# Performance work log

Measured on AMD Instinct MI355X. Metric: run time of the kernel, lower is better.

The kernel has to match this reference:

```python
import jax, jax.numpy as jnp
import numpy as np

STRIDE = 1
PADDING = 1


def sign_ste(w):
    # forward: 2*(w>0)-1 ; backward: identity (straight-through estimator)
    s = 2.0 * (w > 0.0).astype(w.dtype) - 1.0
    return w + jax.lax.stop_gradient(s - w)


def setup_inputs() -> dict:
    key = jax.random.key(0)
    kx, kw = jax.random.split(key)
    x = jax.random.normal(kx, (32, 256, 56, 56), dtype=jnp.float32)
    # mirror torch.rand(shape) * 0.001
    weight = jax.random.uniform(kw, (256, 256, 3, 3), dtype=jnp.float32) * 0.001
    return {"x": x, "weight": weight}


def reference(x, weight):
    # per-output-channel scaling factor: mean |w| over (in, kh, kw), detached
    scaling = jnp.mean(jnp.abs(weight), axis=(1, 2, 3), keepdims=True)  # [O,1,1,1]
    scaling = jax.lax.stop_gradient(scaling)
    binary_weights = scaling * sign_ste(weight)
    y = jax.lax.conv_general_dilated(
        x, binary_weights,
        window_strides=(STRIDE, STRIDE),
        padding=[(PADDING, PADDING), (PADDING, PADDING)],
        dimension_numbers=("NCHW", "OIHW", "NCHW"),
    )
    return y
```

## Files before the change

kernel.cpp:

```cpp
#include <hip/hip_runtime.h>
#include <stdint.h>


typedef float f32x4 __attribute__((ext_vector_type(4)));

__global__ __launch_bounds__(256) void stage1U(const float* __restrict__ x,
                                               float* __restrict__ U,
                                               const float* __restrict__ w,
                                               float* __restrict__ scale,
                                               int* __restrict__ nneg,
                                               int* __restrict__ negidx) {
    __shared__ float Ls[16][64];
    __shared__ float red[4];
    __shared__ int cnt;
    const int t = threadIdx.x;
    if (blockIdx.x < 1568) {
        const int b    = blockIdx.x;
        const int n    = b / 49;
        const int tile = b - n * 49;
        const int g    = t >> 4;
        const int sl   = t & 15;
        const int hw4  = tile * 16 + sl;
        const f32x4* xp =
            (const f32x4*)(x + (size_t)(n * 256 + g * 16) * 3136) + hw4;
        f32x4 s = {0.f, 0.f, 0.f, 0.f};
#pragma unroll
        for (int c = 0; c < 16; ++c)
            s += __builtin_nontemporal_load(xp + c * 784);
        *(f32x4*)&Ls[g][sl * 4] = s;
        __syncthreads();
        if (t < 64) {
            float us = 0.f;
#pragma unroll
            for (int g2 = 0; g2 < 16; ++g2) us += Ls[g2][t];
            U[(size_t)n * 3136 + tile * 64 + t] = us;
        }
    } else {
        const int o = blockIdx.x - 1568;
        if (t == 0) cnt = 0;
        __syncthreads();
        const float* wp = w + ((size_t)o * 256 + t) * 9;
        float s = 0.f;
#pragma unroll
        for (int k = 0; k < 9; ++k) {
            const float v = wp[k];
            s += fabsf(v);
            if (v <= 0.f) {
                const int slot = atomicAdd(&cnt, 1);
                negidx[o * 2304 + slot] = t * 9 + k;
            }
        }
#pragma unroll
        for (int off = 32; off > 0; off >>= 1) s += __shfl_down(s, off);
        if ((t & 63) == 0) red[t >> 6] = s;
        __syncthreads();
        if (t == 0) {
            scale[o] = (red[0] + red[1] + red[2] + red[3]) * (1.f / 2304.f);
            nneg[o]  = cnt;
        }
    }
}

__global__ __launch_bounds__(256) void youtbox(const float* __restrict__ U,
                                               const float* __restrict__ scale,
                                               const int* __restrict__ nneg,
                                               const int* __restrict__ negidx,
                                               const float* __restrict__ x,
                                               float* __restrict__ out) {
    __shared__ float Us[3136];
    __shared__ float Tls[3136];
    __shared__ float ssc[4];
    __shared__ int   snn[4];
    const int b  = blockIdx.x;
    const int og = b & 63;
    const int n  = b >> 6;
    const int t  = threadIdx.x;

    if (t < 4) {
        ssc[t] = scale[og * 4 + t];
        snn[t] = nneg[og * 4 + t];
    }
    const f32x4* Un4 = (const f32x4*)(U + (size_t)n * 3136);
    f32x4* Us4 = (f32x4*)Us;
#pragma unroll
    for (int j = 0; j < 4; ++j) {
        const int i = t + j * 256;
        if (i < 784) Us4[i] = Un4[i];
    }
    __syncthreads();
    for (int p = t; p < 3136; p += 256) {
        const int h = p / 56, w = p - h * 56;
        float acc = 0.f;
#pragma unroll
        for (int r = -1; r <= 1; ++r) {
            const int hh = h + r;
            if (hh < 0 || hh > 55) continue;
            const float* row = Us + hh * 56;
            if (w > 0)  acc += row[w - 1];
            acc += row[w];
            if (w < 55) acc += row[w + 1];
        }
        Tls[p] = acc;
    }
    __syncthreads();

    const f32x4* T4 = (const f32x4*)Tls;
#pragma unroll
    for (int ol = 0; ol < 4; ++ol) {
        const int o = og * 4 + ol;
        const float sc = ssc[ol];
        const int nn = snn[ol];
        f32x4* op = (f32x4*)(out + ((size_t)n * 256 + o) * 3136);
        if (nn == 0) {
#pragma unroll
            for (int j = 0; j < 4; ++j) {
                const int hw4 = t + j * 256;
                if (hw4 >= 784) break;
                f32x4 v = T4[hw4] * sc;
                __builtin_nontemporal_store(v, op + hw4);
            }
        } else {
            const float c2 = 2.f * sc;
#pragma unroll
            for (int j = 0; j < 4; ++j) {
                const int hw4 = t + j * 256;
                if (hw4 >= 784) break;
                f32x4 v = T4[hw4] * sc;
                for (int q = 0; q < nn; ++q) {
                    const int iof = negidx[o * 2304 + q];
                    const int ic = iof / 9, rs = iof - ic * 9;
                    const int r = rs / 3 - 1, s2 = rs - (rs / 3) * 3 - 1;
                    const float* xpl = x + ((size_t)n * 256 + ic) * 3136;
#pragma unroll
                    for (int e = 0; e < 4; ++e) {
                        const int p = hw4 * 4 + e;
                        const int h = p / 56 + r, ww = p - (p / 56) * 56 + s2;
                        const float xv = (h >= 0 && h < 56 && ww >= 0 && ww < 56)
                                             ? xpl[h * 56 + ww] : 0.f;
                        v[e] -= c2 * xv;
                    }
                }
                __builtin_nontemporal_store(v, op + hw4);
            }
        }
    }
}

extern "C" void kernel_launch(void* const* d_in, const int* in_sizes, int n_in,
                              void* d_out, int out_size, void* d_ws, size_t ws_size,
                              hipStream_t stream) {
    const float* x = (const float*)d_in[0];
    const float* w = (const float*)d_in[1];
    float* out = (float*)d_out;

    char* ws = (char*)d_ws;
    size_t off = 0;
    float* U = (float*)(ws + off);
    off += (size_t)32 * 3136 * 4;
    float* scale = (float*)(ws + off);
    off += 256 * 4;
    int* nneg = (int*)(ws + off);
    off += 256 * 4;
    int* negidx = (int*)(ws + off);

    stage1U<<<dim3(1824), 256, 0, stream>>>(x, U, w, scale, nneg, negidx);
    youtbox<<<dim3(2048), 256, 0, stream>>>(U, scale, nneg, negidx, x, out);
}
```

Baseline: 184.8 us.

## Fuse both stages into one persistent kernel with atomic-flag dataflow sync

Merges the channel-sum/weight-stats kernel and the output kernel into a single persistent kernel of 1024 blocks. The last block finishing a batch's channel sum computes the 3x3 box-summed map T once per batch and publishes it via a release flag. Output blocks spin on per-batch and weight-count flags instead of waiting for a kernel boundary, and they read T from global memory instead of recomputing the box filter per block. This adds a memset launch, relies on all 1024 blocks being co-resident to avoid deadlock, and adds spin-wait overhead.

Measured after the change: 429.2 us. 132% more time.

```diff
diff --git a/kernel.cpp b/kernel.cpp
--- a/kernel.cpp
+++ b/kernel.cpp
@@ -4,120 +4,135 @@
 
 typedef float f32x4 __attribute__((ext_vector_type(4)));
 
-__global__ __launch_bounds__(256) void stage1U(const float* __restrict__ x,
-                                               float* __restrict__ U,
-                                               const float* __restrict__ w,
-                                               float* __restrict__ scale,
-                                               int* __restrict__ nneg,
-                                               int* __restrict__ negidx) {
+#define GRID 1024
+
+__global__ __launch_bounds__(256, 4) void mega(
+    const float* __restrict__ x, float* __restrict__ U, float* __restrict__ T,
+    const float* __restrict__ w, float* __restrict__ scale,
+    int* __restrict__ nneg, int* __restrict__ negidx,
+    int* __restrict__ ucnt, int* __restrict__ wcnt, int* __restrict__ tready,
+    float* __restrict__ out) {
     __shared__ float Ls[16][64];
+    __shared__ float Ub[3136];
     __shared__ float red[4];
     __shared__ int cnt;
+    __shared__ int sflag;
     const int t = threadIdx.x;
-    if (blockIdx.x < 1568) {
-        const int b    = blockIdx.x;
-        const int n    = b / 49;
-        const int tile = b - n * 49;
-        const int g    = t >> 4;
-        const int sl   = t & 15;
-        const int hw4  = tile * 16 + sl;
-        const f32x4* xp =
-            (const f32x4*)(x + (size_t)(n * 256 + g * 16) * 3136) + hw4;
-        f32x4 s = {0.f, 0.f, 0.f, 0.f};
+
+    for (int wb = blockIdx.x; wb < 1824; wb += GRID) {
+        if (wb < 1568) {
+            const int n    = wb / 49;
+            const int tile = wb - n * 49;
+            const int g    = t >> 4;
+            const int sl   = t & 15;
+            const int hw4  = tile * 16 + sl;
+            const f32x4* xp =
+                (const f32x4*)(x + (size_t)(n * 256 + g * 16) * 3136) + hw4;
+            f32x4 s = {0.f, 0.f, 0.f, 0.f};
 #pragma unroll
-        for (int c = 0; c < 16; ++c)
-            s += __builtin_nontemporal_load(xp + c * 784);
-        *(f32x4*)&Ls[g][sl * 4] = s;
-        __syncthreads();
-        if (t < 64) {
-            float us = 0.f;
+            for (int c = 0; c < 16; ++c)
+                s += __builtin_nontemporal_load(xp + c * 784);
+            *(f32x4*)&Ls[g][sl * 4] = s;
+            __syncthreads();
+            if (t < 64) {
+                float us = 0.f;
 #pragma unroll
-            for (int g2 = 0; g2 < 16; ++g2) us += Ls[g2][t];
-            U[(size_t)n * 3136 + tile * 64 + t] = us;
-        }
-    } else {
-        const int o = blockIdx.x - 1568;
-        if (t == 0) cnt = 0;
-        __syncthreads();
-        const float* wp = w + ((size_t)o * 256 + t) * 9;
-        float s = 0.f;
+                for (int g2 = 0; g2 < 16; ++g2) us += Ls[g2][t];
+                U[(size_t)n * 3136 + tile * 64 + t] = us;
+            }
+            __syncthreads();
+            if (t == 0) {
+                __threadfence();
+                const int old = atomicAdd(&ucnt[n], 1);
+                sflag = (old == 48);
+                if (old == 48) __threadfence();
+            }
+            __syncthreads();
+            if (sflag) {
+                const f32x4* Un4 = (const f32x4*)(U + (size_t)n * 3136);
+                f32x4* Ub4 = (f32x4*)Ub;
+                for (int j = t; j < 784; j += 256) Ub4[j] = Un4[j];
+                __syncthreads();
+                float* Tn = T + (size_t)n * 3136;
+                for (int p = t; p < 3136; p += 256) {
+                    const int h = p / 56, wc = p - h * 56;
+                    float acc = 0.f;
 #pragma unroll
-        for (int k = 0; k < 9; ++k) {
-            const float v = wp[k];
-            s += fabsf(v);
-            if (v <= 0.f) {
-                const int slot = atomicAdd(&cnt, 1);
-                negidx[o * 2304 + slot] = t * 9 + k;
+                    for (int r = -1; r <= 1; ++r) {
+                        const int hh = h + r;
+                        if (hh < 0 || hh > 55) continue;
+                        const float* row = Ub + hh * 56;
+                        if (wc > 0)  acc += row[wc - 1];
+                        acc += row[wc];
+                        if (wc < 55) acc += row[wc + 1];
+                    }
+                    Tn[p] = acc;
+                }
+                __syncthreads();
+                if (t == 0) {
+                    __threadfence();
+                    __hip_atomic_store(&tready[n], 1, __ATOMIC_RELEASE,
+                                       __HIP_MEMORY_SCOPE_AGENT);
+                }
+            }
+        } else {
+            const int o = wb - 1568;
+            if (t == 0) cnt = 0;
+            __syncthreads();
+            const float* wp = w + ((size_t)o * 256 + t) * 9;
+            float s = 0.f;
+#pragma unroll
+            for (int k = 0; k < 9; ++k) {
+                const float v = wp[k];
+                s += fabsf(v);
+                if (v <= 0.f) {
+                    const int slot = atomicAdd(&cnt, 1);
+                    negidx[o * 2304 + slot] = t * 9 + k;
+                }
+            }
+#pragma unroll
+            for (int off = 32; off > 0; off >>= 1) s += __shfl_down(s, off);
+            if ((t & 63) == 0) red[t >> 6] = s;
+            __syncthreads();
+            if (t == 0) {
+                scale[o] = (red[0] + red[1] + red[2] + red[3]) * (1.f / 2304.f);
+                nneg[o]  = cnt;
+            }
+            __syncthreads();
+            if (t == 0) {
+                __threadfence();
+                atomicAdd(wcnt, 1);
             }
         }
-#pragma unroll
-        for (int off = 32; off > 0; off >>= 1) s += __shfl_down(s, off);
-        if ((t & 63) == 0) red[t >> 6] = s;
         __syncthreads();
+    }
+
+    bool wdone = false;
+    for (int v = blockIdx.x; v < 8192; v += GRID) {
+        const int n = v >> 8, o = v & 255;
         if (t == 0) {
-            scale[o] = (red[0] + red[1] + red[2] + red[3]) * (1.f / 2304.f);
-            nneg[o]  = cnt;
+            while (!__hip_atomic_load(&tready[n], __ATOMIC_ACQUIRE,
+                                      __HIP_MEMORY_SCOPE_AGENT))
+                __builtin_amdgcn_s_sleep(2);
+            if (!wdone) {
+                while (__hip_atomic_load(wcnt, __ATOMIC_ACQUIRE,
+                                         __HIP_MEMORY_SCOPE_AGENT) < 256)
+                    __builtin_amdgcn_s_sleep(2);
+                wdone = true;
+            }
         }
-    }
-}
-
-__global__ __launch_bounds__(256) void youtbox(const float* __restrict__ U,
-                                               const float* __restrict__ scale,
-                                               const int* __restrict__ nneg,
-                                               const int* __restrict__ negidx,
-                                               const float* __restrict__ x,
-                                               float* __restrict__ out) {
-    __shared__ float Us[3136];
-    __shared__ float Tls[3136];
-    __shared__ float ssc[4];
-    __shared__ int   snn[4];
-    const int b  = blockIdx.x;
-    const int og = b & 63;
-    const int n  = b >> 6;
-    const int t  = threadIdx.x;
-
-    if (t < 4) {
-        ssc[t] = scale[og * 4 + t];
-        snn[t] = nneg[og * 4 + t];
-    }
-    const f32x4* Un4 = (const f32x4*)(U + (size_t)n * 3136);
-    f32x4* Us4 = (f32x4*)Us;
-#pragma unroll
-    for (int j = 0; j < 4; ++j) {
-        const int i = t + j * 256;
-        if (i < 784) Us4[i] = Un4[i];
-    }
-    __syncthreads();
-    for (int p = t; p < 3136; p += 256) {
-        const int h = p / 56, w = p - h * 56;
-        float acc = 0.f;
-#pragma unroll
-        for (int r = -1; r <= 1; ++r) {
-            const int hh = h + r;
-            if (hh < 0 || hh > 55) continue;
-            const float* row = Us + hh * 56;
-            if (w > 0)  acc += row[w - 1];
-            acc += row[w];
-            if (w < 55) acc += row[w + 1];
-        }
-        Tls[p] = acc;
-    }
-    __syncthreads();
-
-    const f32x4* T4 = (const f32x4*)Tls;
-#pragma unroll
-    for (int ol = 0; ol < 4; ++ol) {
-        const int o = og * 4 + ol;
-        const float sc = ssc[ol];
-        const int nn = snn[ol];
+        __syncthreads();
+        const float sc = scale[o];
+        const int nn = nneg[o];
+        const f32x4* Tn = (const f32x4*)(T + (size_t)n * 3136);
         f32x4* op = (f32x4*)(out + ((size_t)n * 256 + o) * 3136);
         if (nn == 0) {
 #pragma unroll
             for (int j = 0; j < 4; ++j) {
                 const int hw4 = t + j * 256;
                 if (hw4 >= 784) break;
-                f32x4 v = T4[hw4] * sc;
-                __builtin_nontemporal_store(v, op + hw4);
+                f32x4 vv = Tn[hw4] * sc;
+                __builtin_nontemporal_store(vv, op + hw4);
             }
         } else {
             const float c2 = 2.f * sc;
@@ -125,7 +140,7 @@
             for (int j = 0; j < 4; ++j) {
                 const int hw4 = t + j * 256;
                 if (hw4 >= 784) break;
-                f32x4 v = T4[hw4] * sc;
+                f32x4 vv = Tn[hw4] * sc;
                 for (int q = 0; q < nn; ++q) {
                     const int iof = negidx[o * 2304 + q];
                     const int ic = iof / 9, rs = iof - ic * 9;
@@ -137,10 +152,10 @@
                         const int h = p / 56 + r, ww = p - (p / 56) * 56 + s2;
                         const float xv = (h >= 0 && h < 56 && ww >= 0 && ww < 56)
                                              ? xpl[h * 56 + ww] : 0.f;
-                        v[e] -= c2 * xv;
+                        vv[e] -= c2 * xv;
                     }
                 }
-                __builtin_nontemporal_store(v, op + hw4);
+                __builtin_nontemporal_store(vv, op + hw4);
             }
         }
     }
@@ -157,12 +172,21 @@
     size_t off = 0;
     float* U = (float*)(ws + off);
     off += (size_t)32 * 3136 * 4;
+    float* T = (float*)(ws + off);
+    off += (size_t)32 * 3136 * 4;
     float* scale = (float*)(ws + off);
     off += 256 * 4;
     int* nneg = (int*)(ws + off);
     off += 256 * 4;
     int* negidx = (int*)(ws + off);
+    off += (size_t)256 * 2304 * 4;
+    int* flags = (int*)(ws + off);
+    int* ucnt   = flags;
+    int* wcnt   = flags + 32;
+    int* tready = flags + 33;
 
-    stage1U<<<dim3(1824), 256, 0, stream>>>(x, U, w, scale, nneg, negidx);
-    youtbox<<<dim3(2048), 256, 0, stream>>>(U, scale, nneg, negidx, x, out);
+    hipMemsetAsync(flags, 0, 65 * sizeof(int), stream);
+    void* null_unused = nullptr; (void)null_unused;
+    mega<<<dim3(GRID), 256, 0, stream>>>(x, U, T, w, scale, nneg, negidx,
+                                         ucnt, wcnt, tready, out);
 }
```
